# Kernel optimization log

Hardware: AMD Instinct MI355X
Metric: run time of the kernel (lower is better)

## Reference

```python
import jax, jax.numpy as jnp
import numpy as np

B, TK, N = 32, 2048, 1024  # batch, encoder steps, 2*hidden_dim


def setup_inputs() -> dict:
    key = jax.random.key(0)
    ks = jax.random.split(key, 12)
    s = 0.02
    return {
        "s_t_hat": jax.random.normal(ks[0], (B, N), jnp.float32),
        "h": jax.random.normal(ks[1], (B, TK, N), jnp.float32),
        "enc_padding_mask": jax.random.uniform(ks[2], (B, TK), jnp.float32),
        "coverage": jax.random.uniform(ks[3], (B, TK), jnp.float32),
        "q_h": jax.random.normal(ks[4], (B, TK, N), jnp.float32),
        "W_h": jax.random.normal(ks[5], (N, N), jnp.float32) * s,
        "W_q": jax.random.normal(ks[6], (N, N), jnp.float32) * s,
        "W_c": jax.random.normal(ks[7], (N,), jnp.float32) * s,   # Linear(1, N) weight, squeezed
        "W_d": jax.random.normal(ks[8], (N, N), jnp.float32) * s,  # decode_proj weight
        "b_d": jnp.zeros((N,), jnp.float32),                       # decode_proj bias
        "v_w": jax.random.normal(ks[9], (N,), jnp.float32) * s,    # v: Linear(N, 1) weight, squeezed
    }


def reference(s_t_hat, h, enc_padding_mask, coverage, q_h, W_h, W_q, W_c, W_d, b_d, v_w):
    # projections (Linear: y = x @ W.T)
    enc_feat = jnp.einsum("btn,mn->btm", h, W_h)            # [B,TK,N]
    q_feat = jnp.einsum("btn,mn->btm", q_h, W_q)            # [B,TK,N]
    dec_feat = s_t_hat @ W_d.T + b_d                         # [B,N]
    cov_feat = coverage[..., None] * W_c                     # [B,TK,N]
    att = jnp.tanh(enc_feat + dec_feat[:, None, :] + q_feat + cov_feat)
    scores = jnp.einsum("btn,n->bt", att, v_w)               # [B,TK]
    attn_ = jax.nn.softmax(scores, axis=1) * enc_padding_mask
    attn = attn_ / jnp.sum(attn_, axis=1, keepdims=True)     # renormalized
    c_t = jnp.einsum("bt,btn->bn", attn, h)                  # context vector
    coverage_out = coverage + attn
    return (c_t, attn, coverage_out)
```

## Files before the change

kernel.cpp:

```cpp
#include <hip/hip_runtime.h>
#include <stdint.h>

#define Bsz 32
#define TKs 2048
#define Nf  1024
#define Msz (Bsz*TKs)
#define KTOT 2048

typedef __bf16 bf16x8 __attribute__((ext_vector_type(8)));
typedef float  f32x4  __attribute__((ext_vector_type(4)));
typedef float  f32x16 __attribute__((ext_vector_type(16)));

__device__ __forceinline__ unsigned pack_bf2(float f0, float f1){
  unsigned u0 = __float_as_uint(f0) + 0x8000u;
  unsigned u1 = __float_as_uint(f1) + 0x8000u;
  return __builtin_amdgcn_perm(u1, u0, 0x07060302u);
}

__device__ __forceinline__ float fast_tanh(float x){
  float e = __expf(2.f * x);
  return 1.f - 2.f * __builtin_amdgcn_rcpf(e + 1.f);
}

__device__ __forceinline__ void async16(void* lds, const void* g){
  __builtin_amdgcn_global_load_lds(
      (const __attribute__((address_space(1))) unsigned int*)g,
      (__attribute__((address_space(3))) unsigned int*)lds,
      16, 0, 0);
}

__global__ __launch_bounds__(256) void pack_w_kernel(
    const float* __restrict__ Wh, const float* __restrict__ Wq,
    unsigned short* __restrict__ Wcat)
{
  int idx = (blockIdx.x * 256 + threadIdx.x) * 4;
  int m = idx >> 11;
  int k = idx & 2047;
  const float* src = (k < 1024) ? (Wh + m * 1024 + k) : (Wq + m * 1024 + (k - 1024));
  float4 v = *(const float4*)src;
  uint2 p;
  p.x = pack_bf2(v.x, v.y);
  p.y = pack_bf2(v.z, v.w);
  *(uint2*)(Wcat + idx) = p;
}

__global__ __launch_bounds__(256) void dec_kernel(
    const float* __restrict__ s_t, const float* __restrict__ Wd,
    const float* __restrict__ bd, float* __restrict__ dec)
{
  __shared__ float sv[1024];
  const int b = blockIdx.y;
  const int mbase = blockIdx.x * 64;
  for (int i = threadIdx.x; i < 1024; i += 256) sv[i] = s_t[b * 1024 + i];
  __syncthreads();
  const int wave = threadIdx.x >> 6, lane = threadIdx.x & 63;
  #pragma unroll 4
  for (int i = 0; i < 16; ++i){
    int m = mbase + wave * 16 + i;
    const float4* wr = (const float4*)(Wd + (size_t)m * 1024 + lane * 16);
    const float4* sr = (const float4*)(sv + lane * 16);
    float s = 0.f;
    #pragma unroll
    for (int j = 0; j < 4; ++j){
      float4 w = wr[j], x = sr[j];
      s += w.x * x.x + w.y * x.y + w.z * x.z + w.w * x.w;
    }
    #pragma unroll
    for (int d = 1; d < 64; d <<= 1) s += __shfl_xor(s, d);
    if (lane == 0) dec[b * 1024 + m] = s + bd[m];
  }
}

__global__ __launch_bounds__(256) void gemm_fused_fast(
    const float* __restrict__ h, const float* __restrict__ q,
    const unsigned short* __restrict__ Wcat,
    const float* __restrict__ dec, const float* __restrict__ cov,
    const float* __restrict__ Wc, const float* __restrict__ vw,
    float* __restrict__ scoresP)
{
  __shared__ __align__(16) unsigned short As[128 * 32];
  __shared__ __align__(16) unsigned short Bs[128 * 32];
  __shared__ float ssum[2][128];
  __shared__ float covS[128];

  const int tid  = threadIdx.x;
  const int wave = tid >> 6, lane = tid & 63;
  const int wm = wave & 1, wn = wave >> 1;
  const int l31 = lane & 31, half = lane >> 5;

  const int p = blockIdx.x;
  const int ntile = (p >> 3) & 7;
  const int mtile = (p & 7) + ((p >> 6) << 3);
  const size_t growbase = (size_t)mtile * 128;

  if (tid < 128) covS[tid] = cov[growbase + tid];

  f32x16 acc[2][2];
  #pragma unroll
  for (int i = 0; i < 2; ++i)
    #pragma unroll
    for (int j = 0; j < 2; ++j)
      #pragma unroll
      for (int r = 0; r < 16; ++r) acc[i][j][r] = 0.f;

  const int s0 = wave * 128 + lane;
  const int s1 = s0 + 64;
  const int r0 = s0 >> 2, g0 = (s0 & 3) ^ ((r0 >> 1) & 3);
  const int r1 = s1 >> 2, g1 = (s1 & 3) ^ ((r1 >> 1) & 3);

  const size_t aOff0 = (size_t)(mtile * 128 + r0) * 1024 + g0 * 8;
  const size_t aOff1 = (size_t)(mtile * 128 + r1) * 1024 + g1 * 8;
  unsigned short* stA0 = &As[s0 * 8];
  unsigned short* stA1 = &As[s1 * 8];

  const unsigned short* pB0 = Wcat + (size_t)(ntile * 128 + r0) * 2048 + g0 * 8;
  const unsigned short* pB1 = Wcat + (size_t)(ntile * 128 + r1) * 2048 + g1 * 8;
  unsigned short* ldsB0 = &Bs[wave * 1024];
  unsigned short* ldsB1 = &Bs[wave * 1024 + 512];

  const bf16x8* a_rd[2][2];
  const bf16x8* b_rd[2][2];
  #pragma unroll
  for (int mi = 0; mi < 2; ++mi)
    #pragma unroll
    for (int ks = 0; ks < 2; ++ks){
      int row = wm * 64 + mi * 32 + l31;
      int g = ks * 2 + half;
      int pos = g ^ ((row >> 1) & 3);
      a_rd[mi][ks] = (const bf16x8*)&As[row * 32 + pos * 8];
    }
  #pragma unroll
  for (int ni = 0; ni < 2; ++ni)
    #pragma unroll
    for (int ks = 0; ks < 2; ++ks){
      int row = wn * 64 + ni * 32 + l31;
      int g = ks * 2 + half;
      int pos = g ^ ((row >> 1) & 3);
      b_rd[ni][ks] = (const bf16x8*)&Bs[row * 32 + pos * 8];
    }

  float4 pf00 = *(const float4*)(h + aOff0);
  float4 pf01 = *(const float4*)(h + aOff0 + 4);
  float4 pf10 = *(const float4*)(h + aOff1);
  float4 pf11 = *(const float4*)(h + aOff1 + 4);

  for (int kt = 0; kt < KTOT / 32; ++kt){
    uint4 w0, w1;
    w0.x = pack_bf2(pf00.x, pf00.y); w0.y = pack_bf2(pf00.z, pf00.w);
    w0.z = pack_bf2(pf01.x, pf01.y); w0.w = pack_bf2(pf01.z, pf01.w);
    w1.x = pack_bf2(pf10.x, pf10.y); w1.y = pack_bf2(pf10.z, pf10.w);
    w1.z = pack_bf2(pf11.x, pf11.y); w1.w = pack_bf2(pf11.z, pf11.w);
    *(uint4*)stA0 = w0;
    *(uint4*)stA1 = w1;
    async16(ldsB0, pB0);
    async16(ldsB1, pB1);
    pB0 += 32; pB1 += 32;
    __syncthreads();

    if (kt < KTOT / 32 - 1){
      int c = ((kt + 1) * 32) & 1023;
      const float* sp = (kt + 1 < 32) ? h : q;
      pf00 = *(const float4*)(sp + aOff0 + c);
      pf01 = *(const float4*)(sp + aOff0 + c + 4);
      pf10 = *(const float4*)(sp + aOff1 + c);
      pf11 = *(const float4*)(sp + aOff1 + c + 4);
    }

    bf16x8 af[2][2], bg[2][2];
    #pragma unroll
    for (int i = 0; i < 2; ++i)
      #pragma unroll
      for (int ks = 0; ks < 2; ++ks){ af[i][ks] = *a_rd[i][ks]; bg[i][ks] = *b_rd[i][ks]; }
    #pragma unroll
    for (int ks = 0; ks < 2; ++ks)
      #pragma unroll
      for (int mi = 0; mi < 2; ++mi)
        #pragma unroll
        for (int ni = 0; ni < 2; ++ni)
          acc[mi][ni] = __builtin_amdgcn_mfma_f32_32x32x16_bf16(
              af[mi][ks], bg[ni][ks], acc[mi][ni], 0, 0, 0);
    __syncthreads();
  }

  const int brow = (mtile * 128) >> 11;
  const float* decb = dec + brow * 1024;
  float dv[2], wc2[2], vw2[2];
  #pragma unroll
  for (int ni = 0; ni < 2; ++ni){
    int col = ntile * 128 + wn * 64 + ni * 32 + l31;
    dv[ni]  = decb[col];
    wc2[ni] = Wc[col];
    vw2[ni] = vw[col];
  }
  #pragma unroll
  for (int mi = 0; mi < 2; ++mi){
    #pragma unroll
    for (int r = 0; r < 16; ++r){
      int rl = wm * 64 + mi * 32 + (r & 3) + 8 * (r >> 2) + 4 * half;
      float cv = covS[rl];
      float s = 0.f;
      #pragma unroll
      for (int ni = 0; ni < 2; ++ni){
        float x = acc[mi][ni][r] + dv[ni] + cv * wc2[ni];
        s += vw2[ni] * fast_tanh(x);
      }
      #pragma unroll
      for (int d = 1; d < 32; d <<= 1) s += __shfl_xor(s, d);
      if (l31 == 0) ssum[wn][rl] = s;
    }
  }
  __syncthreads();
  if (tid < 128)
    scoresP[(size_t)ntile * Msz + growbase + tid] = ssum[0][tid] + ssum[1][tid];
}

__global__ __launch_bounds__(256) void softmax_kernel(
    const float* __restrict__ scoresP, const float* __restrict__ mask,
    const float* __restrict__ cov, float* __restrict__ attn_o,
    float* __restrict__ cov_o)
{
  const int b = blockIdx.x;
  const int tid = threadIdx.x;
  const int wave = tid >> 6, lane = tid & 63;
  __shared__ float redm[4], reds[4];
  float sc[8];
  float mx = -3.4e38f;
  #pragma unroll
  for (int j = 0; j < 8; ++j){
    int t = tid + j * 256;
    float s = 0.f;
    #pragma unroll
    for (int p = 0; p < 8; ++p) s += scoresP[(size_t)p * Msz + b * TKs + t];
    sc[j] = s;
    mx = fmaxf(mx, s);
  }
  #pragma unroll
  for (int d = 1; d < 64; d <<= 1) mx = fmaxf(mx, __shfl_xor(mx, d));
  if (lane == 0) redm[wave] = mx;
  __syncthreads();
  mx = fmaxf(fmaxf(redm[0], redm[1]), fmaxf(redm[2], redm[3]));
  float e[8]; float sum = 0.f;
  #pragma unroll
  for (int j = 0; j < 8; ++j){
    int t = tid + j * 256;
    float v = __expf(sc[j] - mx) * mask[b * TKs + t];
    e[j] = v; sum += v;
  }
  #pragma unroll
  for (int d = 1; d < 64; d <<= 1) sum += __shfl_xor(sum, d);
  if (lane == 0) reds[wave] = sum;
  __syncthreads();
  sum = reds[0] + reds[1] + reds[2] + reds[3];
  float inv = 1.f / sum;
  #pragma unroll
  for (int j = 0; j < 8; ++j){
    int t = tid + j * 256;
    float a = e[j] * inv;
    attn_o[b * TKs + t] = a;
    cov_o[b * TKs + t]  = cov[b * TKs + t] + a;
  }
}

__global__ __launch_bounds__(256) void ct_partial(
    const float* __restrict__ h, const float* __restrict__ attn,
    float* __restrict__ P)
{
  const int b = blockIdx.y, tc = blockIdx.x;
  const int n4 = threadIdx.x * 4;
  float4 acc = {0.f, 0.f, 0.f, 0.f};
  const float* hb = h + ((size_t)b * TKs + tc * 64) * Nf;
  const float* ab = attn + b * TKs + tc * 64;
  #pragma unroll 4
  for (int tt = 0; tt < 64; ++tt){
    float a = ab[tt];
    float4 hv = *(const float4*)(hb + (size_t)tt * Nf + n4);
    acc.x += a * hv.x; acc.y += a * hv.y; acc.z += a * hv.z; acc.w += a * hv.w;
  }
  *(float4*)(P + ((size_t)(tc * Bsz + b)) * Nf + n4) = acc;
}

__global__ __launch_bounds__(256) void ct_reduce(
    const float* __restrict__ P, float* __restrict__ out)
{
  int bn = (blockIdx.x * 256 + threadIdx.x) * 4;
  float4 s = {0.f, 0.f, 0.f, 0.f};
  for (int j = 0; j < 32; ++j){
    float4 v = *(const float4*)(P + (size_t)j * (Bsz * Nf) + bn);
    s.x += v.x; s.y += v.y; s.z += v.z; s.w += v.w;
  }
  *(float4*)(out + bn) = s;
}

extern "C" void kernel_launch(void* const* d_in, const int* in_sizes, int n_in,
                              void* d_out, int out_size, void* d_ws, size_t ws_size,
                              hipStream_t stream) {
  const float* s_t  = (const float*)d_in[0];
  const float* h    = (const float*)d_in[1];
  const float* mask = (const float*)d_in[2];
  const float* cov  = (const float*)d_in[3];
  const float* qh   = (const float*)d_in[4];
  const float* Wh   = (const float*)d_in[5];
  const float* Wq   = (const float*)d_in[6];
  const float* Wc   = (const float*)d_in[7];
  const float* Wd   = (const float*)d_in[8];
  const float* bd   = (const float*)d_in[9];
  const float* vw   = (const float*)d_in[10];

  float* out    = (float*)d_out;
  float* c_t    = out;
  float* attn_o = out + Bsz * Nf;
  float* cov_o  = attn_o + Bsz * TKs;

  char* ws = (char*)d_ws;
  unsigned short* Wcat = (unsigned short*)ws;
  float* dec     = (float*)(ws + (4u << 20));
  float* scoresP = (float*)(ws + (4u << 20) + (128u << 10));
  float* ctP     = (float*)(ws + (6u << 20) + (128u << 10));

  hipLaunchKernelGGL(pack_w_kernel, dim3(2048), dim3(256), 0, stream, Wh, Wq, Wcat);
  hipLaunchKernelGGL(dec_kernel,    dim3(16, 32), dim3(256), 0, stream, s_t, Wd, bd, dec);
  hipLaunchKernelGGL(gemm_fused_fast, dim3(4096), dim3(256), 0, stream,
                     h, qh, Wcat, dec, cov, Wc, vw, scoresP);
  hipLaunchKernelGGL(softmax_kernel, dim3(32), dim3(256), 0, stream,
                     scoresP, mask, cov, attn_o, cov_o);
  hipLaunchKernelGGL(ct_partial, dim3(32, 32), dim3(256), 0, stream, h, attn_o, ctP);
  hipLaunchKernelGGL(ct_reduce,  dim3(32), dim3(256), 0, stream, ctP, c_t);
}
```

Measured before the change: 996.2 us.

## Pre-pack activations to bf16 and use larger double-buffered async GEMM tiles

A new pass converts h and q_h to one concatenated bf16 matrix up front. The fused GEMM then streams both operands straight into LDS with async loads. The GEMM tile grows to 256x256 with 512 threads and a BK=64 double buffer, with split LDS reads, priority hints and explicit waitcnt/barrier scheduling. This should raise MFMA utilisation and halve the scoresP partials. The context-vector pass now reads bf16 h instead of fp32, which lowers c_t precision. The extra pack pass writes and reads a 256MB buffer, which costs traffic.

```diff
diff --git a/kernel.cpp b/kernel.cpp
--- a/kernel.cpp
+++ b/kernel.cpp
@@ -8,7 +8,6 @@
 #define KTOT 2048
 
 typedef __bf16 bf16x8 __attribute__((ext_vector_type(8)));
-typedef float  f32x4  __attribute__((ext_vector_type(4)));
 typedef float  f32x16 __attribute__((ext_vector_type(16)));
 
 __device__ __forceinline__ unsigned pack_bf2(float f0, float f1){
@@ -42,6 +41,22 @@
   p.x = pack_bf2(v.x, v.y);
   p.y = pack_bf2(v.z, v.w);
   *(uint2*)(Wcat + idx) = p;
+}
+
+__global__ __launch_bounds__(256) void pack_a_kernel(
+    const float* __restrict__ h, const float* __restrict__ q,
+    unsigned short* __restrict__ Acat)
+{
+  size_t idx = ((size_t)blockIdx.x * 256 + threadIdx.x) * 8;
+  size_t r = idx >> 11;
+  int c = (int)(idx & 2047);
+  const float* src = (c < 1024) ? (h + r * 1024 + c) : (q + r * 1024 + (c - 1024));
+  float4 v0 = ((const float4*)src)[0];
+  float4 v1 = ((const float4*)src)[1];
+  uint4 p;
+  p.x = pack_bf2(v0.x, v0.y); p.y = pack_bf2(v0.z, v0.w);
+  p.z = pack_bf2(v1.x, v1.y); p.w = pack_bf2(v1.z, v1.w);
+  *(uint4*)(Acat + idx) = p;
 }
 
 __global__ __launch_bounds__(256) void dec_kernel(
@@ -71,147 +86,154 @@
   }
 }
 
-__global__ __launch_bounds__(256) void gemm_fused_fast(
-    const float* __restrict__ h, const float* __restrict__ q,
+__global__ __launch_bounds__(512, 2) void gemm_fused_fast(
+    const unsigned short* __restrict__ Acat,
     const unsigned short* __restrict__ Wcat,
     const float* __restrict__ dec, const float* __restrict__ cov,
     const float* __restrict__ Wc, const float* __restrict__ vw,
     float* __restrict__ scoresP)
 {
-  __shared__ __align__(16) unsigned short As[128 * 32];
-  __shared__ __align__(16) unsigned short Bs[128 * 32];
-  __shared__ float ssum[2][128];
-  __shared__ float covS[128];
+  __shared__ __align__(16) unsigned short As[2 * 256 * 64];
+  __shared__ __align__(16) unsigned short Bs[2 * 256 * 64];
 
   const int tid  = threadIdx.x;
-  const int wave = tid >> 6, lane = tid & 63;
-  const int wm = wave & 1, wn = wave >> 1;
-  const int l31 = lane & 31, half = lane >> 5;
-
-  const int p = blockIdx.x;
-  const int ntile = (p >> 3) & 7;
-  const int mtile = (p & 7) + ((p >> 6) << 3);
-  const size_t growbase = (size_t)mtile * 128;
-
-  if (tid < 128) covS[tid] = cov[growbase + tid];
-
-  f32x16 acc[2][2];
-  #pragma unroll
-  for (int i = 0; i < 2; ++i)
-    #pragma unroll
-    for (int j = 0; j < 2; ++j)
-      #pragma unroll
-      for (int r = 0; r < 16; ++r) acc[i][j][r] = 0.f;
-
-  const int s0 = wave * 128 + lane;
-  const int s1 = s0 + 64;
-  const int r0 = s0 >> 2, g0 = (s0 & 3) ^ ((r0 >> 1) & 3);
-  const int r1 = s1 >> 2, g1 = (s1 & 3) ^ ((r1 >> 1) & 3);
-
-  const size_t aOff0 = (size_t)(mtile * 128 + r0) * 1024 + g0 * 8;
-  const size_t aOff1 = (size_t)(mtile * 128 + r1) * 1024 + g1 * 8;
-  unsigned short* stA0 = &As[s0 * 8];
-  unsigned short* stA1 = &As[s1 * 8];
-
-  const unsigned short* pB0 = Wcat + (size_t)(ntile * 128 + r0) * 2048 + g0 * 8;
-  const unsigned short* pB1 = Wcat + (size_t)(ntile * 128 + r1) * 2048 + g1 * 8;
-  unsigned short* ldsB0 = &Bs[wave * 1024];
-  unsigned short* ldsB1 = &Bs[wave * 1024 + 512];
-
-  const bf16x8* a_rd[2][2];
-  const bf16x8* b_rd[2][2];
-  #pragma unroll
-  for (int mi = 0; mi < 2; ++mi)
-    #pragma unroll
-    for (int ks = 0; ks < 2; ++ks){
-      int row = wm * 64 + mi * 32 + l31;
-      int g = ks * 2 + half;
-      int pos = g ^ ((row >> 1) & 3);
-      a_rd[mi][ks] = (const bf16x8*)&As[row * 32 + pos * 8];
-    }
-  #pragma unroll
-  for (int ni = 0; ni < 2; ++ni)
-    #pragma unroll
-    for (int ks = 0; ks < 2; ++ks){
-      int row = wn * 64 + ni * 32 + l31;
-      int g = ks * 2 + half;
-      int pos = g ^ ((row >> 1) & 3);
-      b_rd[ni][ks] = (const bf16x8*)&Bs[row * 32 + pos * 8];
-    }
-
-  float4 pf00 = *(const float4*)(h + aOff0);
-  float4 pf01 = *(const float4*)(h + aOff0 + 4);
-  float4 pf10 = *(const float4*)(h + aOff1);
-  float4 pf11 = *(const float4*)(h + aOff1 + 4);
-
-  for (int kt = 0; kt < KTOT / 32; ++kt){
-    uint4 w0, w1;
-    w0.x = pack_bf2(pf00.x, pf00.y); w0.y = pack_bf2(pf00.z, pf00.w);
-    w0.z = pack_bf2(pf01.x, pf01.y); w0.w = pack_bf2(pf01.z, pf01.w);
-    w1.x = pack_bf2(pf10.x, pf10.y); w1.y = pack_bf2(pf10.z, pf10.w);
-    w1.z = pack_bf2(pf11.x, pf11.y); w1.w = pack_bf2(pf11.z, pf11.w);
-    *(uint4*)stA0 = w0;
-    *(uint4*)stA1 = w1;
-    async16(ldsB0, pB0);
-    async16(ldsB1, pB1);
-    pB0 += 32; pB1 += 32;
-    __syncthreads();
-
-    if (kt < KTOT / 32 - 1){
-      int c = ((kt + 1) * 32) & 1023;
-      const float* sp = (kt + 1 < 32) ? h : q;
-      pf00 = *(const float4*)(sp + aOff0 + c);
-      pf01 = *(const float4*)(sp + aOff0 + c + 4);
-      pf10 = *(const float4*)(sp + aOff1 + c);
-      pf11 = *(const float4*)(sp + aOff1 + c + 4);
-    }
-
-    bf16x8 af[2][2], bg[2][2];
-    #pragma unroll
-    for (int i = 0; i < 2; ++i)
-      #pragma unroll
-      for (int ks = 0; ks < 2; ++ks){ af[i][ks] = *a_rd[i][ks]; bg[i][ks] = *b_rd[i][ks]; }
+  const int l    = tid & 63, w = tid >> 6;
+  const int wm   = w & 1, wn = w >> 1;
+  const int l31  = l & 31, half = l >> 5;
+
+  const int bid   = blockIdx.x;
+  const int orig  = (bid & 7) * 128 + (bid >> 3);
+  const int mtile = orig >> 2;
+  const int ntile = orig & 3;
+
+  f32x16 acc[4][2];
+  #pragma unroll
+  for (int mi = 0; mi < 4; ++mi)
+    #pragma unroll
+    for (int ni = 0; ni < 2; ++ni)
+      #pragma unroll
+      for (int r = 0; r < 16; ++r) acc[mi][ni][r] = 0.f;
+
+  const int t8  = tid >> 3;
+  const int kgS = (tid & 7) ^ (t8 & 7);
+  const unsigned short* aS = Acat + (size_t)(mtile * 256 + t8) * 2048 + kgS * 8;
+  const unsigned short* bS = Wcat + (size_t)(ntile * 256 + t8) * 2048 + kgS * 8;
+
+#define STAGE(bsel, kt_) do {                                                   \
+    _Pragma("unroll")                                                           \
+    for (int j = 0; j < 4; ++j) {                                               \
+      async16(&As[(bsel) * 16384 + j * 4096 + w * 512],                         \
+              aS + (size_t)(kt_) * 64 + (size_t)j * 131072);                    \
+      async16(&Bs[(bsel) * 16384 + j * 4096 + w * 512],                         \
+              bS + (size_t)(kt_) * 64 + (size_t)j * 131072);                    \
+    }                                                                           \
+  } while (0)
+
+  const int aRow = (wm * 128 + l31) * 64;
+  const int bRow = (wn * 64  + l31) * 64;
+  int kgx[4];
+  #pragma unroll
+  for (int ks = 0; ks < 4; ++ks) kgx[ks] = (((ks * 2 + half) ^ (l & 7))) * 8;
+
+  STAGE(0, 0);
+  STAGE(1, 1);
+  asm volatile("s_waitcnt vmcnt(8)" ::: "memory");
+  __builtin_amdgcn_s_barrier();
+
+  for (int kt = 0; kt < 32; ++kt){
+    const int bo = (kt & 1) * 16384;
+    bf16x8 aF[4][2], bF[2][2];
+    #pragma unroll
+    for (int mi = 0; mi < 4; ++mi)
+      #pragma unroll
+      for (int ks = 0; ks < 2; ++ks)
+        aF[mi][ks] = *(const bf16x8*)&As[bo + aRow + mi * 2048 + kgx[ks]];
+    #pragma unroll
+    for (int ni = 0; ni < 2; ++ni)
+      #pragma unroll
+      for (int ks = 0; ks < 2; ++ks)
+        bF[ni][ks] = *(const bf16x8*)&Bs[bo + bRow + ni * 2048 + kgx[ks]];
+    __builtin_amdgcn_s_setprio(1);
     #pragma unroll
     for (int ks = 0; ks < 2; ++ks)
       #pragma unroll
-      for (int mi = 0; mi < 2; ++mi)
+      for (int mi = 0; mi < 4; ++mi)
         #pragma unroll
         for (int ni = 0; ni < 2; ++ni)
           acc[mi][ni] = __builtin_amdgcn_mfma_f32_32x32x16_bf16(
-              af[mi][ks], bg[ni][ks], acc[mi][ni], 0, 0, 0);
-    __syncthreads();
-  }
-
-  const int brow = (mtile * 128) >> 11;
+              aF[mi][ks], bF[ni][ks], acc[mi][ni], 0, 0, 0);
+    __builtin_amdgcn_s_setprio(0);
+    bf16x8 aG[4][2], bG[2][2];
+    #pragma unroll
+    for (int mi = 0; mi < 4; ++mi)
+      #pragma unroll
+      for (int ks = 0; ks < 2; ++ks)
+        aG[mi][ks] = *(const bf16x8*)&As[bo + aRow + mi * 2048 + kgx[2 + ks]];
+    #pragma unroll
+    for (int ni = 0; ni < 2; ++ni)
+      #pragma unroll
+      for (int ks = 0; ks < 2; ++ks)
+        bG[ni][ks] = *(const bf16x8*)&Bs[bo + bRow + ni * 2048 + kgx[2 + ks]];
+    asm volatile("s_waitcnt lgkmcnt(0)" ::: "memory");
+    __builtin_amdgcn_sched_barrier(0);
+    __builtin_amdgcn_s_barrier();
+    __builtin_amdgcn_sched_barrier(0);
+    if (kt < 30) STAGE(kt & 1, kt + 2);
+    __builtin_amdgcn_s_setprio(1);
+    #pragma unroll
+    for (int ks = 0; ks < 2; ++ks)
+      #pragma unroll
+      for (int mi = 0; mi < 4; ++mi)
+        #pragma unroll
+        for (int ni = 0; ni < 2; ++ni)
+          acc[mi][ni] = __builtin_amdgcn_mfma_f32_32x32x16_bf16(
+              aG[mi][ks], bG[ni][ks], acc[mi][ni], 0, 0, 0);
+    __builtin_amdgcn_s_setprio(0);
+    if (kt < 30) { asm volatile("s_waitcnt vmcnt(8)" ::: "memory"); }
+    else         { asm volatile("s_waitcnt vmcnt(0)" ::: "memory"); }
+    __builtin_amdgcn_s_barrier();
+  }
+#undef STAGE
+
+  float* ssum = (float*)As;
+  const size_t growbase = (size_t)mtile * 256;
+  const int brow = mtile >> 3;
   const float* decb = dec + brow * 1024;
   float dv[2], wc2[2], vw2[2];
   #pragma unroll
   for (int ni = 0; ni < 2; ++ni){
-    int col = ntile * 128 + wn * 64 + ni * 32 + l31;
+    int col = ntile * 256 + wn * 64 + ni * 32 + l31;
     dv[ni]  = decb[col];
     wc2[ni] = Wc[col];
     vw2[ni] = vw[col];
   }
   #pragma unroll
-  for (int mi = 0; mi < 2; ++mi){
-    #pragma unroll
-    for (int r = 0; r < 16; ++r){
-      int rl = wm * 64 + mi * 32 + (r & 3) + 8 * (r >> 2) + 4 * half;
-      float cv = covS[rl];
-      float s = 0.f;
-      #pragma unroll
-      for (int ni = 0; ni < 2; ++ni){
-        float x = acc[mi][ni][r] + dv[ni] + cv * wc2[ni];
-        s += vw2[ni] * fast_tanh(x);
+  for (int mi = 0; mi < 4; ++mi){
+    #pragma unroll
+    for (int rq = 0; rq < 4; ++rq){
+      const int rbase = wm * 128 + mi * 32 + 8 * rq + 4 * half;
+      float4 cvv = *(const float4*)&cov[growbase + rbase];
+      #pragma unroll
+      for (int rb = 0; rb < 4; ++rb){
+        const int r = rq * 4 + rb;
+        float cv = (&cvv.x)[rb];
+        float s = 0.f;
+        #pragma unroll
+        for (int ni = 0; ni < 2; ++ni){
+          float x = acc[mi][ni][r] + dv[ni] + cv * wc2[ni];
+          s += vw2[ni] * fast_tanh(x);
+        }
+        #pragma unroll
+        for (int d = 1; d < 32; d <<= 1) s += __shfl_xor(s, d);
+        if (l31 == 0) ssum[wn * 256 + rbase + rb] = s;
       }
-      #pragma unroll
-      for (int d = 1; d < 32; d <<= 1) s += __shfl_xor(s, d);
-      if (l31 == 0) ssum[wn][rl] = s;
     }
   }
-  __syncthreads();
-  if (tid < 128)
-    scoresP[(size_t)ntile * Msz + growbase + tid] = ssum[0][tid] + ssum[1][tid];
+  asm volatile("s_waitcnt lgkmcnt(0)" ::: "memory");
+  __builtin_amdgcn_s_barrier();
+  if (tid < 256)
+    scoresP[(size_t)ntile * Msz + growbase + tid] =
+        ssum[tid] + ssum[256 + tid] + ssum[512 + tid] + ssum[768 + tid];
 }
 
 __global__ __launch_bounds__(256) void softmax_kernel(
@@ -230,7 +252,7 @@
     int t = tid + j * 256;
     float s = 0.f;
     #pragma unroll
-    for (int p = 0; p < 8; ++p) s += scoresP[(size_t)p * Msz + b * TKs + t];
+    for (int p = 0; p < 4; ++p) s += scoresP[(size_t)p * Msz + b * TKs + t];
     sc[j] = s;
     mx = fmaxf(mx, s);
   }
@@ -261,22 +283,25 @@
   }
 }
 
-__global__ __launch_bounds__(256) void ct_partial(
-    const float* __restrict__ h, const float* __restrict__ attn,
+__global__ __launch_bounds__(256) void ct_partial_bf(
+    const unsigned short* __restrict__ Acat, const float* __restrict__ attn,
     float* __restrict__ P)
 {
   const int b = blockIdx.y, tc = blockIdx.x;
-  const int n4 = threadIdx.x * 4;
+  const int c4 = threadIdx.x * 4;
   float4 acc = {0.f, 0.f, 0.f, 0.f};
-  const float* hb = h + ((size_t)b * TKs + tc * 64) * Nf;
+  const size_t rbase = (size_t)b * TKs + tc * 64;
   const float* ab = attn + b * TKs + tc * 64;
   #pragma unroll 4
   for (int tt = 0; tt < 64; ++tt){
     float a = ab[tt];
-    float4 hv = *(const float4*)(hb + (size_t)tt * Nf + n4);
-    acc.x += a * hv.x; acc.y += a * hv.y; acc.z += a * hv.z; acc.w += a * hv.w;
-  }
-  *(float4*)(P + ((size_t)(tc * Bsz + b)) * Nf + n4) = acc;
+    uint2 v = *(const uint2*)(Acat + (rbase + tt) * 2048 + c4);
+    acc.x += a * __uint_as_float(v.x << 16);
+    acc.y += a * __uint_as_float(v.x & 0xffff0000u);
+    acc.z += a * __uint_as_float(v.y << 16);
+    acc.w += a * __uint_as_float(v.y & 0xffff0000u);
+  }
+  *(float4*)(P + ((size_t)(tc * Bsz + b)) * Nf + c4) = acc;
 }
 
 __global__ __launch_bounds__(256) void ct_reduce(
@@ -316,13 +341,16 @@
   float* dec     = (float*)(ws + (4u << 20));
   float* scoresP = (float*)(ws + (4u << 20) + (128u << 10));
   float* ctP     = (float*)(ws + (6u << 20) + (128u << 10));
+  unsigned short* Acat = (unsigned short*)(ws + (16ull << 20));
 
   hipLaunchKernelGGL(pack_w_kernel, dim3(2048), dim3(256), 0, stream, Wh, Wq, Wcat);
   hipLaunchKernelGGL(dec_kernel,    dim3(16, 32), dim3(256), 0, stream, s_t, Wd, bd, dec);
-  hipLaunchKernelGGL(gemm_fused_fast, dim3(4096), dim3(256), 0, stream,
-                     h, qh, Wcat, dec, cov, Wc, vw, scoresP);
+  hipLaunchKernelGGL(pack_a_kernel, dim3((unsigned)((size_t)Msz * KTOT / 8 / 256)),
+                     dim3(256), 0, stream, h, qh, Acat);
+  hipLaunchKernelGGL(gemm_fused_fast, dim3(1024), dim3(512), 0, stream,
+                     Acat, Wcat, dec, cov, Wc, vw, scoresP);
   hipLaunchKernelGGL(softmax_kernel, dim3(32), dim3(256), 0, stream,
                      scoresP, mask, cov, attn_o, cov_o);
-  hipLaunchKernelGGL(ct_partial, dim3(32, 32), dim3(256), 0, stream, h, attn_o, ctP);
+  hipLaunchKernelGGL(ct_partial_bf, dim3(32, 32), dim3(256), 0, stream, Acat, attn_o, ctP);
   hipLaunchKernelGGL(ct_reduce,  dim3(32), dim3(256), 0, stream, ctP, c_t);
 }
```

After: 937.6 us. 1.06x faster.
